# Kernel optimization log

Hardware: AMD Instinct MI355X
Metric: run time of the kernel (lower is better)

The kernel has to match this reference:

```python
import jax, jax.numpy as jnp
import numpy as np

LAMBDA_VOLUME = 0.2
LAMBDA_WEIGHTED_ADJ = 0.15
LAMBDA_SYM = 0.05
AGE_MAX = 100.0
EPS_ROW = 1e-8
EPS_STD = 1e-6


def _smooth_l1(x):
    # F.smooth_l1_loss(x, 0) with beta=1, mean reduction
    ax = jnp.abs(x)
    return jnp.mean(jnp.where(ax < 1.0, 0.5 * x * x, ax - 0.5))


def setup_inputs() -> dict:
    key = jax.random.key(0)
    ks = jax.random.split(key, 9)
    B, C, X = 2, 32, 96
    logits = jax.random.normal(ks[0], (B, C, X, X, X), dtype=jnp.float32)
    age = jax.random.uniform(ks[1], (B, 1), dtype=jnp.float32) * AGE_MAX
    w_young = jax.random.uniform(ks[2], (C, C), dtype=jnp.float32)
    w_old = jax.random.uniform(ks[3], (C, C), dtype=jnp.float32)
    # expected per-class volumes ~ total_voxels / C in scale
    vol_means_young = jax.random.uniform(ks[4], (C,), dtype=jnp.float32) * 50000.0
    vol_means_old = jax.random.uniform(ks[5], (C,), dtype=jnp.float32) * 50000.0
    vol_stds_young = jax.random.uniform(ks[6], (C,), dtype=jnp.float32) * 5000.0 + 1000.0
    vol_stds_old = jax.random.uniform(ks[7], (C,), dtype=jnp.float32) * 5000.0 + 1000.0
    prior_adj = jax.random.uniform(ks[8], (C, C), dtype=jnp.float32)
    # left-right pair permutation: class i <-> i + C//2
    perm = jnp.concatenate([jnp.arange(C // 2, C), jnp.arange(0, C // 2)]).astype(jnp.int64)
    return {"logits": logits, "age": age, "w_young": w_young, "w_old": w_old,
            "vol_means_young": vol_means_young, "vol_means_old": vol_means_old,
            "vol_stds_young": vol_stds_young, "vol_stds_old": vol_stds_old,
            "prior_adj": prior_adj, "perm": perm}


def reference(logits, age, w_young, w_old, vol_means_young, vol_means_old,
              vol_stds_young, vol_stds_old, prior_adj, perm):
    B, C = logits.shape[0], logits.shape[1]
    probs = jax.nn.softmax(logits, axis=1)  # (B,C,X,Y,Z)
    alpha = jnp.clip(age / AGE_MAX, 0.0, 1.0)  # (B,1) interpolation between age anchors

    # ---- weighted adjacency loss (temperature == 1.0 -> no pow) ----
    pf = probs.reshape(B, C, -1)                     # (B,C,N)
    A = jnp.einsum('bcn,bdn->bcd', pf, pf)           # bmm(probs, probs^T)
    A = A * (1.0 - jnp.eye(C, dtype=A.dtype))        # zero diagonal
    W = (1.0 - alpha)[:, :, None] * w_young[None] + alpha[:, :, None] * w_old[None]  # (B,C,C)
    A = A * W
    Aw = A.mean(axis=0)
    Aw = Aw / jnp.clip(Aw.sum(axis=1, keepdims=True), EPS_ROW)
    prior = prior_adj * (1.0 - jnp.eye(C, dtype=prior_adj.dtype))
    prior = prior / jnp.clip(prior.sum(axis=1, keepdims=True), EPS_ROW)
    loss_adj = jnp.mean(jnp.abs(Aw - prior))

    # ---- volume consistency loss ----
    pred_vol = probs.sum(axis=(2, 3, 4))             # (B,C)
    means = (1.0 - alpha) * vol_means_young[None] + alpha * vol_means_old[None]
    stds = (1.0 - alpha) * vol_stds_young[None] + alpha * vol_stds_old[None]
    loss_vol = _smooth_l1((pred_vol - means) / (stds + EPS_STD))

    # ---- symmetry consistency loss (flip along X axis = dim 2, swap LR pairs) ----
    p_flip = jnp.flip(probs, axis=2)
    p_swap = p_flip[:, perm]                         # channel permutation = pairwise swap
    loss_sym = jnp.mean(jnp.abs(probs - p_swap))

    total = (LAMBDA_WEIGHTED_ADJ * loss_adj
             + LAMBDA_VOLUME * loss_vol
             + LAMBDA_SYM * loss_sym)
    return total
```

## Files before the change

kernel.cpp:

```cpp
#include <hip/hip_runtime.h>
#include <math.h>

#define CX 32
#define XX 9216
#define X3 884736
#define CHUNKS_PER_B 13824
#define NBLOCKS 1024
#define WPB 1024

typedef short s8v __attribute__((ext_vector_type(8)));
typedef float f32x16 __attribute__((ext_vector_type(16)));

__device__ __forceinline__ unsigned bf16rne(float f) {
    unsigned u = __float_as_uint(f);
    return (u + (0x7fffu + ((u >> 16) & 1u))) >> 16;
}

__device__ __forceinline__ void gload_lds16(const float* g, float* l) {
    __builtin_amdgcn_global_load_lds(
        (const __attribute__((address_space(1))) void*)g,
        (__attribute__((address_space(3))) void*)l, 16, 0, 0);
}


__global__ __launch_bounds__(128, 2)
void main_pass(const float* __restrict__ logits,
               float* __restrict__ A_acc,
               float* __restrict__ sym_acc)
{
    __shared__ __align__(16) float lds_f[10240];
    const int tid = threadIdx.x;
    const int w   = tid >> 6;
    const int l   = tid & 63;
    const int wid = blockIdx.x * 2 + w;
    const int b   = wid >> 10;
    const int wb  = wid & 1023;
    const int lane31 = l & 31;
    const int h = l >> 5;

    float* const stA = lds_f + w * 4096;
    float* const stB = stA + 2048;
    unsigned char* const sbB = (unsigned char*)(lds_f + 8192 + w * 1024);
    const float* lg = logits + (size_t)b * (size_t)(CX * X3);

    const int ci0   = l >> 4;
    const int pos   = (l & 15) * 4;
    const int posm  = pos & 31;
    const int phalf = pos >> 5;

    const int trips = (wb < 512) ? 14 : 13;

    f32x16 acc = {};
    float sym = 0.f;
    float p[CX];

    auto stage = [&](float* buf, int cg) {
        int x  = cg / 288;
        int rb = (cg - x * 288) * 32;
        int xx = phalf ? (95 - x) : x;
        const float* gp = lg + (size_t)ci0 * X3 + (size_t)xx * XX + (rb + posm);
#pragma unroll
        for (int i = 0; i < 8; ++i)
            gload_lds16(gp + (size_t)i * (size_t)(4 * X3), buf + i * 256);
    };

    stage(stA, wb);
    for (int it = 0; it < trips; ++it) {
        float* cur = (it & 1) ? stB : stA;
        float* nxt = (it & 1) ? stA : stB;
        if (it + 1 < trips) {
            stage(nxt, wb + (it + 1) * WPB);
            __builtin_amdgcn_sched_barrier(0);
            asm volatile("s_waitcnt vmcnt(8)" ::: "memory");
            __builtin_amdgcn_sched_barrier(0);
        } else {
            __builtin_amdgcn_sched_barrier(0);
            asm volatile("s_waitcnt vmcnt(0)" ::: "memory");
            __builtin_amdgcn_sched_barrier(0);
        }

#pragma unroll
        for (int c = 0; c < CX; ++c) p[c] = cur[c * 64 + l];
        float mx[16];
#pragma unroll
        for (int c = 0; c < 16; ++c) mx[c] = fmaxf(p[c], p[c + 16]);
#pragma unroll
        for (int s = 8; s >= 1; s >>= 1)
#pragma unroll
            for (int c = 0; c < s; ++c) mx[c] = fmaxf(mx[c], mx[c + s]);
        float m = mx[0];
        float s0 = 0.f, s1 = 0.f, s2 = 0.f, s3 = 0.f;
#pragma unroll
        for (int c = 0; c < CX; c += 4) {
            p[c]     = __expf(p[c]     - m);
            p[c + 1] = __expf(p[c + 1] - m);
            p[c + 2] = __expf(p[c + 2] - m);
            p[c + 3] = __expf(p[c + 3] - m);
            s0 += p[c]; s1 += p[c + 1]; s2 += p[c + 2]; s3 += p[c + 3];
        }
        float inv = 1.f / ((s0 + s1) + (s2 + s3));
#pragma unroll
        for (int c = 0; c < CX; ++c) p[c] *= inv;

#pragma unroll
        for (int c = 0; c < CX; ++c) {
            int byte = c * 128 + ((2 * l) ^ ((c & 7) << 4));
            *(unsigned short*)(sbB + byte) = (unsigned short)bf16rne(p[c]);
        }

        __builtin_amdgcn_sched_barrier(0);
        asm volatile("s_waitcnt lgkmcnt(0)" ::: "memory");
        __builtin_amdgcn_sched_barrier(0);

#pragma unroll
        for (int c = 0; c < CX; ++c) {
            int cc = (c + 16) & 31;
            int byte = cc * 128 + ((2 * (l ^ 32)) ^ ((cc & 7) << 4));
            unsigned q = *(const unsigned short*)(sbB + byte);
            sym += fabsf(p[c] - __uint_as_float(q << 16));
        }

#pragma unroll
        for (int t = 0; t < 4; ++t) {
            int byte = lane31 * 128 + ((32 * t + 16 * h) ^ ((lane31 & 7) << 4));
            s8v af = *(const s8v*)(sbB + byte);
            acc = __builtin_amdgcn_mfma_f32_32x32x16_bf16(af, af, acc, 0, 0, 0);
        }
    }

    __syncthreads();
#pragma unroll
    for (int r = 0; r < 16; ++r) {
        int row = (r & 3) + 8 * (r >> 2) + 4 * h;
        lds_f[w * 1024 + row * 32 + lane31] = acc[r];
    }
    float sv = sym;
#pragma unroll
    for (int o = 32; o >= 1; o >>= 1) sv += __shfl_down(sv, o);
    if (l == 0) lds_f[2048 + w] = sv;
    __syncthreads();

    {
        const float4* f4 = (const float4*)lds_f;
        float4 u0 = f4[2 * tid],     v0 = f4[2 * tid + 256];
        float4 u1 = f4[2 * tid + 1], v1 = f4[2 * tid + 257];
        float* Ab = A_acc + b * (CX * CX) + tid * 8;
        atomicAdd(&Ab[0], u0.x + v0.x);
        atomicAdd(&Ab[1], u0.y + v0.y);
        atomicAdd(&Ab[2], u0.z + v0.z);
        atomicAdd(&Ab[3], u0.w + v0.w);
        atomicAdd(&Ab[4], u1.x + v1.x);
        atomicAdd(&Ab[5], u1.y + v1.y);
        atomicAdd(&Ab[6], u1.z + v1.z);
        atomicAdd(&Ab[7], u1.w + v1.w);
    }
    if (tid == 0)
        atomicAdd(sym_acc, lds_f[2048] + lds_f[2049]);
}

__global__ void finalize(const float* __restrict__ A_acc,
                         const float* __restrict__ sym,
                         const float* __restrict__ age,
                         const float* __restrict__ wy,  const float* __restrict__ wo,
                         const float* __restrict__ vmy, const float* __restrict__ vmo,
                         const float* __restrict__ vsy, const float* __restrict__ vso,
                         const float* __restrict__ prior,
                         float* __restrict__ out)
{
    const int t = threadIdx.x;
    float a0 = fminf(fmaxf(age[0] * 0.01f, 0.f), 1.f);
    float a1 = fminf(fmaxf(age[1] * 0.01f, 0.f), 1.f);

    const int bb = t >> 5, c = t & 31;
    float full = 0.f;
#pragma unroll
    for (int d = 0; d < CX; ++d) full += A_acc[bb * 1024 + c * CX + d];

    float part_vol;
    {
        float al = bb ? a1 : a0;
        float mean = (1.f - al) * vmy[c] + al * vmo[c];
        float sd   = (1.f - al) * vsy[c] + al * vso[c] + 1e-6f;
        float r  = (full - mean) / sd;
        float ar = fabsf(r);
        part_vol = (ar < 1.f) ? 0.5f * r * r : (ar - 0.5f);
    }

    float part_adj = 0.f;
    if (t < 32) {
        float awrow[CX], prow[CX];
        float rs = 0.f, ps = 0.f;
#pragma unroll
        for (int d = 0; d < CX; ++d) {
            float v = 0.f, pv = 0.f;
            if (d != c) {
                float A0v = A_acc[c * CX + d];
                float A1v = A_acc[1024 + c * CX + d];
                float w0 = (1.f - a0) * wy[c * CX + d] + a0 * wo[c * CX + d];
                float w1 = (1.f - a1) * wy[c * CX + d] + a1 * wo[c * CX + d];
                v  = 0.5f * (A0v * w0 + A1v * w1);
                pv = prior[c * CX + d];
            }
            awrow[d] = v;  rs += v;
            prow[d]  = pv; ps += pv;
        }
        rs = fmaxf(rs, 1e-8f);
        ps = fmaxf(ps, 1e-8f);
#pragma unroll
        for (int d = 0; d < CX; ++d)
            part_adj += fabsf(awrow[d] / rs - prow[d] / ps);
    }

#pragma unroll
    for (int off = 32; off >= 1; off >>= 1) {
        part_adj += __shfl_down(part_adj, off);
        part_vol += __shfl_down(part_vol, off);
    }
    if (t == 0) {
        float loss_adj = part_adj * (1.f / 1024.f);
        float loss_vol = part_vol * (1.f / 64.f);
        float loss_sym = sym[0] / 56623104.f;
        out[0] = 0.15f * loss_adj + 0.2f * loss_vol + 0.05f * loss_sym;
    }
}

extern "C" void kernel_launch(void* const* d_in, const int* in_sizes, int n_in,
                              void* d_out, int out_size, void* d_ws, size_t ws_size,
                              hipStream_t stream) {
    const float* logits = (const float*)d_in[0];
    const float* age    = (const float*)d_in[1];
    const float* wy     = (const float*)d_in[2];
    const float* wo     = (const float*)d_in[3];
    const float* vmy    = (const float*)d_in[4];
    const float* vmo    = (const float*)d_in[5];
    const float* vsy    = (const float*)d_in[6];
    const float* vso    = (const float*)d_in[7];
    const float* prior  = (const float*)d_in[8];

    float* ws    = (float*)d_ws;
    float* A_acc = ws;
    float* sym   = ws + 2048;

    hipMemsetAsync(d_ws, 0, 2049 * sizeof(float), stream);
    main_pass<<<NBLOCKS, 128, 0, stream>>>(logits, A_acc, sym);
    finalize<<<1, 64, 0, stream>>>(A_acc, sym, age, wy, wo,
                                   vmy, vmo, vsy, vso, prior, (float*)d_out);
}
```

Baseline: 436.1 us.

## Restructure main pass into 256-thread blocks sharing staged tiles across waves

Reorganizes the main pass so each 256-thread block handles a fixed x-slice and its mirrored slice, with four waves cooperatively staging contiguous 512-byte rows through LDS and exchanging mirrored probabilities between waves. The grid grows to 1728 blocks with a fixed four trips each, replacing the uneven per-wave trip counts and the scattered 64-byte strided loads. Global loads become more contiguous and the load is balanced evenly. The cost is block-level barriers each iteration and more LDS per block, which may limit occupancy.

```diff
diff --git a/kernel.cpp b/kernel.cpp
--- a/kernel.cpp
+++ b/kernel.cpp
@@ -4,9 +4,9 @@
 #define CX 32
 #define XX 9216
 #define X3 884736
-#define CHUNKS_PER_B 13824
-#define NBLOCKS 1024
-#define WPB 1024
+#define BLKS_PER_B 864
+#define NBLOCKS 1728
+#define TRIPS 4
 
 typedef short s8v __attribute__((ext_vector_type(8)));
 typedef float f32x16 __attribute__((ext_vector_type(16)));
@@ -23,71 +23,76 @@
 }
 
 
-__global__ __launch_bounds__(128, 2)
+__global__ __launch_bounds__(256, 2)
 void main_pass(const float* __restrict__ logits,
                float* __restrict__ A_acc,
                float* __restrict__ sym_acc)
 {
-    __shared__ __align__(16) float lds_f[10240];
+    __shared__ __align__(16) float lds_f[20480];
     const int tid = threadIdx.x;
     const int w   = tid >> 6;
     const int l   = tid & 63;
-    const int wid = blockIdx.x * 2 + w;
-    const int b   = wid >> 10;
-    const int wb  = wid & 1023;
     const int lane31 = l & 31;
     const int h = l >> 5;
 
-    float* const stA = lds_f + w * 4096;
-    float* const stB = stA + 2048;
-    unsigned char* const sbB = (unsigned char*)(lds_f + 8192 + w * 1024);
+    const int b   = blockIdx.x / BLKS_PER_B;
+    const int blk = blockIdx.x - b * BLKS_PER_B;
+    const int s   = blk / 18;
+    const int q   = blk - s * 18;
+    const int rbase = q * 512;
+
     const float* lg = logits + (size_t)b * (size_t)(CX * X3);
 
-    const int ci0   = l >> 4;
-    const int pos   = (l & 15) * 4;
-    const int posm  = pos & 31;
-    const int phalf = pos >> 5;
-
-    const int trips = (wb < 512) ? 14 : 13;
+    const int side_w = w >> 1;
+    const int vcol   = ((w & 1) << 6) + l;
+
+    unsigned short* const sbT  =
+        (unsigned short*)(lds_f + 16384) + w * 2048;
+    unsigned short* const sbTp =
+        (unsigned short*)(lds_f + 16384) + (w ^ 2) * 2048;
 
     f32x16 acc = {};
     float sym = 0.f;
     float p[CX];
 
-    auto stage = [&](float* buf, int cg) {
-        int x  = cg / 288;
-        int rb = (cg - x * 288) * 32;
-        int xx = phalf ? (95 - x) : x;
-        const float* gp = lg + (size_t)ci0 * X3 + (size_t)xx * XX + (rb + posm);
-#pragma unroll
-        for (int i = 0; i < 8; ++i)
-            gload_lds16(gp + (size_t)i * (size_t)(4 * X3), buf + i * 256);
+    auto stage = [&](int bufk, int t) {
+        float* dst0 = lds_f + bufk * 8192;
+        const int r0 = rbase + t * 128 + 4 * (l & 31);
+#pragma unroll
+        for (int i = 0; i < 8; ++i) {
+            const int side  = i & 1;
+            const int cpair = 8 * w + 2 * (i >> 1);
+            const int c     = cpair + (l >> 5);
+            const int x     = side ? (95 - s) : s;
+            const float* gp = lg + (size_t)c * X3 + (size_t)x * XX + r0;
+            gload_lds16(gp, dst0 + side * 4096 + cpair * 128);
+        }
     };
 
-    stage(stA, wb);
-    for (int it = 0; it < trips; ++it) {
-        float* cur = (it & 1) ? stB : stA;
-        float* nxt = (it & 1) ? stA : stB;
-        if (it + 1 < trips) {
-            stage(nxt, wb + (it + 1) * WPB);
+    stage(0, 0);
+    for (int t = 0; t < TRIPS; ++t) {
+        if (t + 1 < TRIPS) {
+            stage((t + 1) & 1, t + 1);
             __builtin_amdgcn_sched_barrier(0);
             asm volatile("s_waitcnt vmcnt(8)" ::: "memory");
-            __builtin_amdgcn_sched_barrier(0);
         } else {
             __builtin_amdgcn_sched_barrier(0);
             asm volatile("s_waitcnt vmcnt(0)" ::: "memory");
-            __builtin_amdgcn_sched_barrier(0);
-        }
-
-#pragma unroll
-        for (int c = 0; c < CX; ++c) p[c] = cur[c * 64 + l];
+        }
+        __builtin_amdgcn_sched_barrier(0);
+        __builtin_amdgcn_s_barrier();
+        __builtin_amdgcn_sched_barrier(0);
+
+        const float* st = lds_f + (t & 1) * 8192 + side_w * 4096;
+#pragma unroll
+        for (int c = 0; c < CX; ++c) p[c] = st[c * 128 + vcol];
         float mx[16];
 #pragma unroll
         for (int c = 0; c < 16; ++c) mx[c] = fmaxf(p[c], p[c + 16]);
 #pragma unroll
-        for (int s = 8; s >= 1; s >>= 1)
-#pragma unroll
-            for (int c = 0; c < s; ++c) mx[c] = fmaxf(mx[c], mx[c + s]);
+        for (int ss = 8; ss >= 1; ss >>= 1)
+#pragma unroll
+            for (int c = 0; c < ss; ++c) mx[c] = fmaxf(mx[c], mx[c + ss]);
         float m = mx[0];
         float s0 = 0.f, s1 = 0.f, s2 = 0.f, s3 = 0.f;
 #pragma unroll
@@ -103,27 +108,26 @@
         for (int c = 0; c < CX; ++c) p[c] *= inv;
 
 #pragma unroll
-        for (int c = 0; c < CX; ++c) {
-            int byte = c * 128 + ((2 * l) ^ ((c & 7) << 4));
-            *(unsigned short*)(sbB + byte) = (unsigned short)bf16rne(p[c]);
-        }
+        for (int c = 0; c < CX; ++c)
+            sbT[c * 64 + (l ^ ((c & 7) << 3))] = (unsigned short)bf16rne(p[c]);
 
         __builtin_amdgcn_sched_barrier(0);
         asm volatile("s_waitcnt lgkmcnt(0)" ::: "memory");
+        __builtin_amdgcn_sched_barrier(0);
+        __builtin_amdgcn_s_barrier();
         __builtin_amdgcn_sched_barrier(0);
 
 #pragma unroll
         for (int c = 0; c < CX; ++c) {
             int cc = (c + 16) & 31;
-            int byte = cc * 128 + ((2 * (l ^ 32)) ^ ((cc & 7) << 4));
-            unsigned q = *(const unsigned short*)(sbB + byte);
-            sym += fabsf(p[c] - __uint_as_float(q << 16));
-        }
-
-#pragma unroll
-        for (int t = 0; t < 4; ++t) {
-            int byte = lane31 * 128 + ((32 * t + 16 * h) ^ ((lane31 & 7) << 4));
-            s8v af = *(const s8v*)(sbB + byte);
+            unsigned q16 = sbTp[cc * 64 + (l ^ ((cc & 7) << 3))];
+            sym += fabsf(p[c] - __uint_as_float(q16 << 16));
+        }
+
+#pragma unroll
+        for (int tt = 0; tt < 4; ++tt) {
+            const s8v af = *(const s8v*)
+                (sbT + lane31 * 64 + ((16 * tt + 8 * h) ^ ((lane31 & 7) << 3)));
             acc = __builtin_amdgcn_mfma_f32_32x32x16_bf16(af, af, acc, 0, 0, 0);
         }
     }
@@ -137,25 +141,25 @@
     float sv = sym;
 #pragma unroll
     for (int o = 32; o >= 1; o >>= 1) sv += __shfl_down(sv, o);
-    if (l == 0) lds_f[2048 + w] = sv;
+    if (l == 0) lds_f[4096 + w] = sv;
     __syncthreads();
 
     {
-        const float4* f4 = (const float4*)lds_f;
-        float4 u0 = f4[2 * tid],     v0 = f4[2 * tid + 256];
-        float4 u1 = f4[2 * tid + 1], v1 = f4[2 * tid + 257];
-        float* Ab = A_acc + b * (CX * CX) + tid * 8;
-        atomicAdd(&Ab[0], u0.x + v0.x);
-        atomicAdd(&Ab[1], u0.y + v0.y);
-        atomicAdd(&Ab[2], u0.z + v0.z);
-        atomicAdd(&Ab[3], u0.w + v0.w);
-        atomicAdd(&Ab[4], u1.x + v1.x);
-        atomicAdd(&Ab[5], u1.y + v1.y);
-        atomicAdd(&Ab[6], u1.z + v1.z);
-        atomicAdd(&Ab[7], u1.w + v1.w);
+        float4 sum = make_float4(0.f, 0.f, 0.f, 0.f);
+#pragma unroll
+        for (int ww = 0; ww < 4; ++ww) {
+            const float4 v = *((const float4*)lds_f + ww * 256 + tid);
+            sum.x += v.x; sum.y += v.y; sum.z += v.z; sum.w += v.w;
+        }
+        float* Ab = A_acc + b * (CX * CX) + tid * 4;
+        atomicAdd(&Ab[0], sum.x);
+        atomicAdd(&Ab[1], sum.y);
+        atomicAdd(&Ab[2], sum.z);
+        atomicAdd(&Ab[3], sum.w);
     }
     if (tid == 0)
-        atomicAdd(sym_acc, lds_f[2048] + lds_f[2049]);
+        atomicAdd(sym_acc,
+                  lds_f[4096] + lds_f[4097] + lds_f[4098] + lds_f[4099]);
 }
 
 __global__ void finalize(const float* __restrict__ A_acc,
@@ -242,7 +246,7 @@
     float* sym   = ws + 2048;
 
     hipMemsetAsync(d_ws, 0, 2049 * sizeof(float), stream);
-    main_pass<<<NBLOCKS, 128, 0, stream>>>(logits, A_acc, sym);
+    main_pass<<<NBLOCKS, 256, 0, stream>>>(logits, A_acc, sym);
     finalize<<<1, 64, 0, stream>>>(A_acc, sym, age, wy, wo,
                                    vmy, vmo, vsy, vso, prior, (float*)d_out);
 }
```

After: 400.1 us. 8.2% less time.
